# Optimization experiments

Hardware: AMD Instinct MI355X
Metric: run time of the kernel (lower is better)

Reference implementation:

```python
import jax, jax.numpy as jnp
import numpy as np

LEARNING_RATE = 0.005
WEIGHT_DECAY = 0.0001


def setup_inputs() -> dict:
    key = jax.random.key(0)
    k1, k2, k3 = jax.random.split(key, 3)
    B, POST, PRE = 128, 1024, 1024
    pre_spikes = jax.random.uniform(k1, (B, PRE), dtype=jnp.float32)
    post_spikes = jax.random.uniform(k2, (B, POST), dtype=jnp.float32)
    weights = jax.random.normal(k3, (POST, PRE), dtype=jnp.float32)
    return {"pre_spikes": pre_spikes, "post_spikes": post_spikes, "weights": weights}


def reference(pre_spikes, post_spikes, weights):
    # mean over batch of outer products post_b (x) pre_b == post^T @ pre / B
    B = pre_spikes.shape[0]
    mean_hebbian = jnp.einsum('bp,bq->pq', post_spikes, pre_spikes) / B  # (post, pre)
    dw = LEARNING_RATE * (mean_hebbian - WEIGHT_DECAY * weights)
    return dw
```

## Files before the change

kernel.cpp:

```cpp
#include <hip/hip_runtime.h>


constexpr int   KB    = 128;
constexpr int   MPOST = 1024;
constexpr int   NPRE  = 1024;
constexpr int   LSTR  = 68;
constexpr float LR    = 0.005f;
constexpr float WD    = 0.0001f;

__global__ __launch_bounds__(256) void hebb_kernel(
    const float* __restrict__ pre,
    const float* __restrict__ post,
    const float* __restrict__ W,
    float* __restrict__ out)
{
    __shared__ float As[KB * LSTR];
    __shared__ float Bs[KB * LSTR];

    const int tx  = threadIdx.x;
    const int ty  = threadIdx.y;
    const int tid = ty * 16 + tx;
    const int bm  = blockIdx.y * 64;
    const int bn  = blockIdx.x * 64;

    #pragma unroll
    for (int i = 0; i < 8; ++i) {
        const int idx = i * 256 + tid;
        const int row = idx >> 4;
        const int c4  = (idx & 15) * 4;
        const float4 a = *reinterpret_cast<const float4*>(post + row * MPOST + bm + c4);
        const float4 b = *reinterpret_cast<const float4*>(pre  + row * NPRE  + bn + c4);
        *reinterpret_cast<float4*>(&As[row * LSTR + c4]) = a;
        *reinterpret_cast<float4*>(&Bs[row * LSTR + c4]) = b;
    }

    const int ty4 = ty * 4, tx4 = tx * 4;
    float4 wreg[4];
    #pragma unroll
    for (int i = 0; i < 4; ++i)
        wreg[i] = *reinterpret_cast<const float4*>(W + (size_t)(bm + ty4 + i) * NPRE + bn + tx4);

    __syncthreads();

    float acc[4][4] = {};
    #pragma unroll 8
    for (int k = 0; k < KB; ++k) {
        const float4 a = *reinterpret_cast<const float4*>(&As[k * LSTR + ty4]);
        const float4 b = *reinterpret_cast<const float4*>(&Bs[k * LSTR + tx4]);
        const float av[4] = {a.x, a.y, a.z, a.w};
        const float bv[4] = {b.x, b.y, b.z, b.w};
        #pragma unroll
        for (int i = 0; i < 4; ++i)
            #pragma unroll
            for (int j = 0; j < 4; ++j)
                acc[i][j] = fmaf(av[i], bv[j], acc[i][j]);
    }

    const float s1 = LR / (float)KB;
    const float s2 = LR * WD;
    #pragma unroll
    for (int i = 0; i < 4; ++i) {
        float4 o;
        o.x = s1 * acc[i][0] - s2 * wreg[i].x;
        o.y = s1 * acc[i][1] - s2 * wreg[i].y;
        o.z = s1 * acc[i][2] - s2 * wreg[i].z;
        o.w = s1 * acc[i][3] - s2 * wreg[i].w;
        *reinterpret_cast<float4*>(out + (size_t)(bm + ty4 + i) * NPRE + bn + tx4) = o;
    }
}

extern "C" void kernel_launch(void* const* d_in, const int* in_sizes, int n_in,
                              void* d_out, int out_size, void* d_ws, size_t ws_size,
                              hipStream_t stream) {
    const float* pre  = (const float*)d_in[0];
    const float* post = (const float*)d_in[1];
    const float* W    = (const float*)d_in[2];
    float* out = (float*)d_out;

    dim3 grid(NPRE / 64, MPOST / 64);
    dim3 block(16, 16);
    hebb_kernel<<<grid, block, 0, stream>>>(pre, post, W, out);
}
```

Before: 66.00 us.

## Replace FP32 FMA GEMM with bf16 MFMA 32x32 tiles per wavefront

Replaces the scalar FP32 outer-product kernel with a single-wavefront-per-block kernel that converts post/pre inputs to bf16 in LDS and accumulates with mfma_f32_32x32x16_bf16. The tile shrinks to 32x32 with 1024 blocks of 64 threads, and W/out use the MFMA output layout with scalar accesses. This aims to remove the FP32 ALU bottleneck and move the compute onto matrix cores. In exchange, precision drops to bf16 inputs, and output stores are no longer vectorized.

```diff
diff --git a/kernel.cpp b/kernel.cpp
--- a/kernel.cpp
+++ b/kernel.cpp
@@ -1,71 +1,86 @@
 #include <hip/hip_runtime.h>
 
 
-constexpr int   KB    = 128;
-constexpr int   MPOST = 1024;
-constexpr int   NPRE  = 1024;
-constexpr int   LSTR  = 68;
-constexpr float LR    = 0.005f;
-constexpr float WD    = 0.0001f;
+using f32x16 = __attribute__((ext_vector_type(16))) float;
+using short8 = __attribute__((ext_vector_type(8))) short;
 
-__global__ __launch_bounds__(256) void hebb_kernel(
+constexpr int   N    = 1024;
+constexpr int   K    = 128;
+constexpr int   LSTR = 136;
+constexpr float LR   = 0.005f;
+constexpr float WD   = 0.0001f;
+
+__device__ inline unsigned short f2bf(float x) {
+    union { float f; unsigned int u; } c; c.f = x;
+    return (unsigned short)((c.u + 0x7FFFu + ((c.u >> 16) & 1u)) >> 16);
+}
+
+__global__ __launch_bounds__(64) void hebb_mfma(
     const float* __restrict__ pre,
     const float* __restrict__ post,
     const float* __restrict__ W,
     float* __restrict__ out)
 {
-    __shared__ float As[KB * LSTR];
-    __shared__ float Bs[KB * LSTR];
+    __shared__ unsigned short A_lds[32 * LSTR];
+    __shared__ unsigned short B_lds[32 * LSTR];
 
-    const int tx  = threadIdx.x;
-    const int ty  = threadIdx.y;
-    const int tid = ty * 16 + tx;
-    const int bm  = blockIdx.y * 64;
-    const int bn  = blockIdx.x * 64;
+    const int l  = threadIdx.x;
+    const int bm = blockIdx.y * 32;
+    const int bn = blockIdx.x * 32;
+
+    const int m4 = (l & 7) * 4;
+    const int k8 = (l >> 3) * 8;
 
     #pragma unroll
-    for (int i = 0; i < 8; ++i) {
-        const int idx = i * 256 + tid;
-        const int row = idx >> 4;
-        const int c4  = (idx & 15) * 4;
-        const float4 a = *reinterpret_cast<const float4*>(post + row * MPOST + bm + c4);
-        const float4 b = *reinterpret_cast<const float4*>(pre  + row * NPRE  + bn + c4);
-        *reinterpret_cast<float4*>(&As[row * LSTR + c4]) = a;
-        *reinterpret_cast<float4*>(&Bs[row * LSTR + c4]) = b;
+    for (int p = 0; p < 2; ++p) {
+        const int kb = k8 + p * 64;
+        float4 av[8], bv[8];
+        #pragma unroll
+        for (int j = 0; j < 8; ++j) {
+            av[j] = *(const float4*)(post + (size_t)(kb + j) * N + bm + m4);
+            bv[j] = *(const float4*)(pre  + (size_t)(kb + j) * N + bn + m4);
+        }
+        #pragma unroll
+        for (int i = 0; i < 4; ++i) {
+            short8 pa, pb;
+            #pragma unroll
+            for (int j = 0; j < 8; ++j) {
+                const float* fa = (const float*)&av[j];
+                const float* fb = (const float*)&bv[j];
+                pa[j] = (short)f2bf(fa[i]);
+                pb[j] = (short)f2bf(fb[i]);
+            }
+            *(short8*)&A_lds[(m4 + i) * LSTR + kb] = pa;
+            *(short8*)&B_lds[(m4 + i) * LSTR + kb] = pb;
+        }
     }
 
-    const int ty4 = ty * 4, tx4 = tx * 4;
-    float4 wreg[4];
+    const int col   = l & 31;
+    const int rbase = 4 * (l >> 5);
+    float wv[16];
     #pragma unroll
-    for (int i = 0; i < 4; ++i)
-        wreg[i] = *reinterpret_cast<const float4*>(W + (size_t)(bm + ty4 + i) * NPRE + bn + tx4);
+    for (int r = 0; r < 16; ++r) {
+        const int row = (r & 3) + 8 * (r >> 2) + rbase;
+        wv[r] = W[(size_t)(bm + row) * N + bn + col];
+    }
 
     __syncthreads();
 
-    float acc[4][4] = {};
-    #pragma unroll 8
-    for (int k = 0; k < KB; ++k) {
-        const float4 a = *reinterpret_cast<const float4*>(&As[k * LSTR + ty4]);
-        const float4 b = *reinterpret_cast<const float4*>(&Bs[k * LSTR + tx4]);
-        const float av[4] = {a.x, a.y, a.z, a.w};
-        const float bv[4] = {b.x, b.y, b.z, b.w};
-        #pragma unroll
-        for (int i = 0; i < 4; ++i)
-            #pragma unroll
-            for (int j = 0; j < 4; ++j)
-                acc[i][j] = fmaf(av[i], bv[j], acc[i][j]);
+    f32x16 acc = {};
+    const int hh = 8 * (l >> 5);
+    #pragma unroll
+    for (int kk = 0; kk < 8; ++kk) {
+        short8 a = *(const short8*)&A_lds[(l & 31) * LSTR + kk * 16 + hh];
+        short8 b = *(const short8*)&B_lds[(l & 31) * LSTR + kk * 16 + hh];
+        acc = __builtin_amdgcn_mfma_f32_32x32x16_bf16(a, b, acc, 0, 0, 0);
     }
 
-    const float s1 = LR / (float)KB;
+    const float s1 = LR / 128.0f;
     const float s2 = LR * WD;
     #pragma unroll
-    for (int i = 0; i < 4; ++i) {
-        float4 o;
-        o.x = s1 * acc[i][0] - s2 * wreg[i].x;
-        o.y = s1 * acc[i][1] - s2 * wreg[i].y;
-        o.z = s1 * acc[i][2] - s2 * wreg[i].z;
-        o.w = s1 * acc[i][3] - s2 * wreg[i].w;
-        *reinterpret_cast<float4*>(out + (size_t)(bm + ty4 + i) * NPRE + bn + tx4) = o;
+    for (int r = 0; r < 16; ++r) {
+        const int row = (r & 3) + 8 * (r >> 2) + rbase;
+        out[(size_t)(bm + row) * N + bn + col] = s1 * acc[r] - s2 * wv[r];
     }
 }
 
@@ -77,7 +92,7 @@
     const float* W    = (const float*)d_in[2];
     float* out = (float*)d_out;
 
-    dim3 grid(NPRE / 64, MPOST / 64);
-    dim3 block(16, 16);
-    hebb_kernel<<<grid, block, 0, stream>>>(pre, post, W, out);
+    dim3 grid(N / 32, N / 32);
+    dim3 block(64);
+    hebb_mfma<<<grid, block, 0, stream>>>(pre, post, W, out);
 }
```

Result: faster. 63.06 us (-4.5%).
